# Kernel tuning notes

Measured on AMD Instinct MI355X. Metric: run time of the kernel, lower is better.

## Reference

```python
import jax, jax.numpy as jnp
import numpy as np

B, T, E, H = 16, 512, 1024, 512  # batch, seq_len, embedding_size_contactenated, contextualization_size


def setup_inputs() -> dict:
    key = jax.random.key(0)
    ks = jax.random.split(key, 10)
    s = 0.02
    return {
        "context_emb": jax.random.normal(ks[0], (B, T, E), dtype=jnp.float32),
        # coupled-gate LSTM cell: 3 gates (i, j, o); W: [3H, E+H]
        "w_fwd": jax.random.normal(ks[1], (3 * H, E + H), dtype=jnp.float32) * s,
        "b_fwd": jnp.zeros((3 * H,), dtype=jnp.float32),
        "w_bwd": jax.random.normal(ks[2], (3 * H, E + H), dtype=jnp.float32) * s,
        "b_bwd": jnp.zeros((3 * H,), dtype=jnp.float32),
        # learned initial states (xavier-ish), shape [1, H] each
        "h0_fwd": jax.random.normal(ks[3], (1, H), dtype=jnp.float32) * s,
        "h0_bwd": jax.random.normal(ks[4], (1, H), dtype=jnp.float32) * s,
        "c0_fwd": jax.random.normal(ks[5], (1, H), dtype=jnp.float32) * s,
        "c0_bwd": jax.random.normal(ks[6], (1, H), dtype=jnp.float32) * s,
    }


def _run_dir(x, w, b, h0, c0):
    # x: [T, B, E]; w: [3H, E+H]; h0, c0: [B, H]
    def step(carry, xt):
        h, c = carry
        gates = jnp.concatenate([xt, h], axis=-1) @ w.T + b  # [B, 3H]
        i, j, o = jnp.split(gates, 3, axis=-1)
        i = jax.nn.sigmoid(i)
        c = (1.0 - i) * c + i * jnp.tanh(j)  # coupled input/forget gate
        h = jnp.tanh(c) * jax.nn.sigmoid(o)
        return (h, c), h

    _, ys = jax.lax.scan(step, (h0, c0), x)
    return ys  # [T, B, H]


def reference(context_emb, w_fwd, b_fwd, w_bwd, b_bwd, h0_fwd, h0_bwd, c0_fwd, c0_bwd):
    x = jnp.transpose(context_emb, (1, 0, 2))  # [T, B, E] (time-major)
    batch = x.shape[1]
    rep = lambda s: jnp.tile(s, (batch, 1))  # repeat learned init state over batch
    out_f = _run_dir(x, w_fwd, b_fwd, rep(h0_fwd), rep(c0_fwd))
    out_b = _run_dir(x[::-1], w_bwd, b_bwd, rep(h0_bwd), rep(c0_bwd))[::-1]
    out = jnp.concatenate([out_f, out_b], axis=-1)  # [T, B, 2H]
    # dropout is identity in eval mode
    return jnp.transpose(out, (1, 0, 2))  # [B, T, 2H]
```

## Files before the change

kernel.cpp:

```cpp
#include <hip/hip_runtime.h>
#include <hip/hip_bf16.h>


typedef __attribute__((ext_vector_type(8))) short s8v;
typedef __attribute__((ext_vector_type(4))) short s4v;
typedef __attribute__((ext_vector_type(4))) float f4v;
typedef __attribute__((ext_vector_type(4))) unsigned short us4;
typedef unsigned long long u64;
typedef unsigned int u32;

#define XBF_OFF   0ull
#define WXBF_OFF  16777216ull
#define WHBF_OFF  23068672ull
#define XG_OFF    26214400ull
#define HST_OFF   76546048ull
#define TAG_OFF   76677120ull

static __device__ __forceinline__ short f2bf(float f) {
  __hip_bfloat16 h = __float2bfloat16(f);
  return *reinterpret_cast<short*>(&h);
}
static __device__ __forceinline__ float bf2f(unsigned short u) {
  union { unsigned int i; float f; } x;
  x.i = ((unsigned int)u) << 16;
  return x.f;
}
static __device__ __forceinline__ float sigmoidf_(float x) {
  return 1.0f / (1.0f + __expf(-x));
}
static __device__ __forceinline__ float tanhf_(float x) {
  return 1.0f - 2.0f / (1.0f + __expf(2.0f * x));
}

__global__ void init_state(const float* __restrict__ h0f, const float* __restrict__ h0b,
                           short* __restrict__ hst, u32* __restrict__ tags) {
  int i = blockIdx.x * 256 + threadIdx.x;
  if (i < 2 * 16 * 512) {
    int dir = i >> 13;
    int r = i & 8191;
    int col = r & 511;
    const float* h0 = dir ? h0b : h0f;
    hst[(size_t)dir * 4 * 8192 + r] = f2bf(h0[col]);
  }
  if (i < 64) tags[i] = 0;
}

__global__ void cast_x(const float* __restrict__ x, short* __restrict__ xb) {
  int i = (blockIdx.x * 256 + threadIdx.x) * 4;
  f4v v = *reinterpret_cast<const f4v*>(x + i);
  s4v o;
#pragma unroll
  for (int j = 0; j < 4; ++j) o[j] = f2bf(v[j]);
  *reinterpret_cast<s4v*>(xb + i) = o;
}

__global__ void cast_w(const float* __restrict__ wf, const float* __restrict__ wb,
                       short* __restrict__ wxb, short* __restrict__ whb) {
  int e = blockIdx.x * 256 + threadIdx.x;
  int dir = blockIdx.y;
  const float* w = dir ? wb : wf;
  int n = e / 1536;
  int k = e - n * 1536;
  short v = f2bf(w[e]);
  if (k < 1024)
    wxb[((size_t)(dir * 1536 + n)) * 1024 + k] = v;
  else
    whb[((size_t)(dir * 1536 + n)) * 512 + (k - 1024)] = v;
}

__global__ __launch_bounds__(256) void gemm_in(const short* __restrict__ Xb,
                                               const short* __restrict__ Wxb,
                                               short* __restrict__ Xg) {
  __shared__ short As[128 * 72];
  __shared__ short Bs[128 * 72];
  int tid = threadIdx.x;
  int lane = tid & 63;
  int lr = lane & 15, quad = lane >> 4;
  int widx = tid >> 6;
  int wr = widx >> 1, wc = widx & 1;
  int bm = blockIdx.x, bn = blockIdx.y;

  f4v acc[4][4];
#pragma unroll
  for (int a = 0; a < 4; ++a)
#pragma unroll
    for (int b = 0; b < 4; ++b) acc[a][b] = {0.f, 0.f, 0.f, 0.f};

  const short* Arow = Xb + (size_t)bm * 128 * 1024;
  const short* Brow = Wxb + (size_t)bn * 128 * 1024;

  for (int kt = 0; kt < 16; ++kt) {
#pragma unroll
    for (int c = 0; c < 4; ++c) {
      int fl = c * 2048 + tid * 8;
      int row = fl >> 6, col = fl & 63;
      *reinterpret_cast<s8v*>(&As[row * 72 + col]) =
          *reinterpret_cast<const s8v*>(Arow + row * 1024 + kt * 64 + col);
      *reinterpret_cast<s8v*>(&Bs[row * 72 + col]) =
          *reinterpret_cast<const s8v*>(Brow + row * 1024 + kt * 64 + col);
    }
    __syncthreads();
#pragma unroll
    for (int kk = 0; kk < 2; ++kk) {
      s8v af[4], bfv[4];
#pragma unroll
      for (int mi = 0; mi < 4; ++mi)
        af[mi] = *reinterpret_cast<const s8v*>(&As[(wr * 64 + mi * 16 + lr) * 72 + kk * 32 + quad * 8]);
#pragma unroll
      for (int ni = 0; ni < 4; ++ni)
        bfv[ni] = *reinterpret_cast<const s8v*>(&Bs[(wc * 64 + ni * 16 + lr) * 72 + kk * 32 + quad * 8]);
#pragma unroll
      for (int mi = 0; mi < 4; ++mi)
#pragma unroll
        for (int ni = 0; ni < 4; ++ni)
          acc[mi][ni] = __builtin_amdgcn_mfma_f32_16x16x32_bf16(af[mi], bfv[ni], acc[mi][ni], 0, 0, 0);
    }
    __syncthreads();
  }

  int ngbase = bn * 128;
  int dir = (ngbase >= 1536) ? 1 : 0;
  int ng0 = ngbase - dir * 1536;
#pragma unroll
  for (int mi = 0; mi < 4; ++mi) {
#pragma unroll
    for (int ni = 0; ni < 4; ++ni) {
      int colg = ng0 + wc * 64 + ni * 16 + lr;
#pragma unroll
      for (int r = 0; r < 4; ++r) {
        int m = bm * 128 + wr * 64 + mi * 16 + quad * 4 + r;
        int b = m >> 9, t = m & 511;
        Xg[(((size_t)(dir * 512 + t)) * 1536 + colg) * 16 + b] = f2bf(acc[mi][ni][r]);
      }
    }
  }
}

__global__ __launch_bounds__(64, 1) void lstm_rec(
    const short* __restrict__ Whb, const short* __restrict__ Xg,
    const float* __restrict__ bfw, const float* __restrict__ bbw,
    const float* __restrict__ c0f, const float* __restrict__ c0b,
    short* __restrict__ hst, u32* __restrict__ tags, float* __restrict__ out) {
  int lane = threadIdx.x & 63;
  int lr = lane & 15, quad = lane >> 4;
  int wg = blockIdx.x;
  int dir = wg >> 5;
  int slice = wg & 31;
  int col16 = slice * 16;

  const short* Whd = Whb + (size_t)dir * 1536 * 512;
  s8v Bw[3][16];
#pragma unroll
  for (int g = 0; g < 3; ++g) {
    const short* rp = Whd + (size_t)(g * 512 + col16 + lr) * 512 + quad * 8;
#pragma unroll
    for (int k = 0; k < 16; ++k) Bw[g][k] = *reinterpret_cast<const s8v*>(rp + k * 32);
  }

  const float* bias = dir ? bbw : bfw;
  float bi = bias[col16 + lr];
  float bj = bias[512 + col16 + lr];
  float bo = bias[1024 + col16 + lr];

  const float* c0 = dir ? c0b : c0f;
  float cst[4];
  {
    float c0v = c0[col16 + lr];
#pragma unroll
    for (int r = 0; r < 4; ++r) cst[r] = c0v;
  }

  short* hring = hst + (size_t)dir * 4 * 8192;
  u32* tg = tags + dir * 32;
  const short* xgbase = Xg + (size_t)dir * 512 * 1536 * 16;

  int t0 = dir ? 511 : 0;
  const short* xgp = xgbase + (size_t)t0 * 1536 * 16;
  us4 xiv = *reinterpret_cast<const us4*>(xgp + (col16 + lr) * 16 + quad * 4);
  us4 xjv = *reinterpret_cast<const us4*>(xgp + (512 + col16 + lr) * 16 + quad * 4);
  us4 xov = *reinterpret_cast<const us4*>(xgp + (1024 + col16 + lr) * 16 + quad * 4);

  for (int s = 0; s < 512; ++s) {
    int t = dir ? (511 - s) : s;

    for (;;) {
      int tv = (int)__hip_atomic_load(&tg[lane & 31], __ATOMIC_RELAXED,
                                      __HIP_MEMORY_SCOPE_AGENT);
      if (__ballot(tv >= s) == ~0ull) break;
    }

    const char* hp = (const char*)(hring + (size_t)(s & 3) * 8192) + lr * 1024 + quad * 16;
    s8v d0, d1, d2, d3, d4, d5, d6, d7, d8, d9, d10, d11, d12, d13, d14, d15;
    asm volatile(
        "global_load_dwordx4 %0, %16, off sc0 sc1\n\t"
        "global_load_dwordx4 %1, %16, off offset:64 sc0 sc1\n\t"
        "global_load_dwordx4 %2, %16, off offset:128 sc0 sc1\n\t"
        "global_load_dwordx4 %3, %16, off offset:192 sc0 sc1\n\t"
        "global_load_dwordx4 %4, %16, off offset:256 sc0 sc1\n\t"
        "global_load_dwordx4 %5, %16, off offset:320 sc0 sc1\n\t"
        "global_load_dwordx4 %6, %16, off offset:384 sc0 sc1\n\t"
        "global_load_dwordx4 %7, %16, off offset:448 sc0 sc1\n\t"
        "global_load_dwordx4 %8, %16, off offset:512 sc0 sc1\n\t"
        "global_load_dwordx4 %9, %16, off offset:576 sc0 sc1\n\t"
        "global_load_dwordx4 %10, %16, off offset:640 sc0 sc1\n\t"
        "global_load_dwordx4 %11, %16, off offset:704 sc0 sc1\n\t"
        "global_load_dwordx4 %12, %16, off offset:768 sc0 sc1\n\t"
        "global_load_dwordx4 %13, %16, off offset:832 sc0 sc1\n\t"
        "global_load_dwordx4 %14, %16, off offset:896 sc0 sc1\n\t"
        "global_load_dwordx4 %15, %16, off offset:960 sc0 sc1\n\t"
        "s_waitcnt vmcnt(0)"
        : "=v"(d0), "=v"(d1), "=v"(d2), "=v"(d3), "=v"(d4), "=v"(d5),
          "=v"(d6), "=v"(d7), "=v"(d8), "=v"(d9), "=v"(d10), "=v"(d11),
          "=v"(d12), "=v"(d13), "=v"(d14), "=v"(d15)
        : "v"(hp)
        : "memory");

    f4v a0 = {0.f, 0.f, 0.f, 0.f};
    f4v a1 = {0.f, 0.f, 0.f, 0.f};
    f4v a2 = {0.f, 0.f, 0.f, 0.f};
    s8v av[16] = {d0, d1, d2, d3, d4, d5, d6, d7, d8, d9, d10, d11, d12, d13, d14, d15};
#pragma unroll
    for (int k = 0; k < 16; ++k) {
      a0 = __builtin_amdgcn_mfma_f32_16x16x32_bf16(av[k], Bw[0][k], a0, 0, 0, 0);
      a1 = __builtin_amdgcn_mfma_f32_16x16x32_bf16(av[k], Bw[1][k], a1, 0, 0, 0);
      a2 = __builtin_amdgcn_mfma_f32_16x16x32_bf16(av[k], Bw[2][k], a2, 0, 0, 0);
    }

    float hn[4];
    u32 hv[4];
#pragma unroll
    for (int r = 0; r < 4; ++r) {
      float gi = a0[r] + bf2f(xiv[r]) + bi;
      float gj = a1[r] + bf2f(xjv[r]) + bj;
      float go = a2[r] + bf2f(xov[r]) + bo;
      float ii = sigmoidf_(gi);
      float jt = tanhf_(gj);
      float oo = sigmoidf_(go);
      cst[r] = (1.0f - ii) * cst[r] + ii * jt;
      hn[r] = tanhf_(cst[r]) * oo;
      hv[r] = (u32)(unsigned short)f2bf(hn[r]);
    }

    {
      short* hd = hring + (size_t)((s + 1) & 3) * 8192;
      const short* hsp = hd + (quad * 4) * 512 + col16 + lr;
      asm volatile(
          "global_store_short %4, %0, off sc0 sc1\n\t"
          "global_store_short %4, %1, off offset:1024 sc0 sc1\n\t"
          "global_store_short %4, %2, off offset:2048 sc0 sc1\n\t"
          "global_store_short %4, %3, off offset:3072 sc0 sc1\n\t"
          "s_waitcnt vmcnt(0)"
          :: "v"(hv[0]), "v"(hv[1]), "v"(hv[2]), "v"(hv[3]), "v"(hsp)
          : "memory");
      if (lane == 0)
        __hip_atomic_store(&tg[slice], (u32)(s + 1), __ATOMIC_RELAXED,
                           __HIP_MEMORY_SCOPE_AGENT);
    }

#pragma unroll
    for (int r = 0; r < 4; ++r)
      out[((size_t)(quad * 4 + r) * 512 + t) * 1024 + dir * 512 + col16 + lr] = hn[r];

    if (s < 511) {
      int tn = dir ? (511 - (s + 1)) : (s + 1);
      const short* xgn = xgbase + (size_t)tn * 1536 * 16;
      xiv = *reinterpret_cast<const us4*>(xgn + (col16 + lr) * 16 + quad * 4);
      xjv = *reinterpret_cast<const us4*>(xgn + (512 + col16 + lr) * 16 + quad * 4);
      xov = *reinterpret_cast<const us4*>(xgn + (1024 + col16 + lr) * 16 + quad * 4);
    }
  }
}

extern "C" void kernel_launch(void* const* d_in, const int* in_sizes, int n_in,
                              void* d_out, int out_size, void* d_ws, size_t ws_size,
                              hipStream_t stream) {
  const float* x    = (const float*)d_in[0];
  const float* wfw  = (const float*)d_in[1];
  const float* bfw  = (const float*)d_in[2];
  const float* wbw  = (const float*)d_in[3];
  const float* bbw  = (const float*)d_in[4];
  const float* h0f  = (const float*)d_in[5];
  const float* h0b  = (const float*)d_in[6];
  const float* c0f  = (const float*)d_in[7];
  const float* c0b  = (const float*)d_in[8];
  float* out = (float*)d_out;

  unsigned char* ws = (unsigned char*)d_ws;
  short* Xbf  = (short*)(ws + XBF_OFF);
  short* Wxbf = (short*)(ws + WXBF_OFF);
  short* Whbf = (short*)(ws + WHBF_OFF);
  short* Xg   = (short*)(ws + XG_OFF);
  short* hst  = (short*)(ws + HST_OFF);
  u32*   tags = (u32*)(ws + TAG_OFF);

  init_state<<<64, 256, 0, stream>>>(h0f, h0b, hst, tags);
  cast_x<<<8192, 256, 0, stream>>>(x, Xbf);
  cast_w<<<dim3(9216, 2), 256, 0, stream>>>(wfw, wbw, Wxbf, Whbf);
  gemm_in<<<dim3(64, 24), 256, 0, stream>>>(Xbf, Wxbf, Xg);
  lstm_rec<<<64, 64, 0, stream>>>(Whbf, Xg, bfw, bbw, c0f, c0b, hst, tags, out);
}
```

Before: 1.812 ms.

## Replace tag-based step barrier with step-stamped hidden-state words

Each bf16 hidden value is now stored in a 32-bit word whose high half carries the step number. Consumers poll the hidden-state buffer directly until every word shows the expected step, which removes the separate tag store, the tag polling loop and the store waitcnt. The ring shrinks from four buffers to two. In exchange, each poll reads twice as many bytes and unpacks them into MFMA operands, and correctness relies on each 32-bit store being atomic.

```diff
diff --git a/kernel.cpp b/kernel.cpp
--- a/kernel.cpp
+++ b/kernel.cpp
@@ -6,6 +6,7 @@
 typedef __attribute__((ext_vector_type(4))) short s4v;
 typedef __attribute__((ext_vector_type(4))) float f4v;
 typedef __attribute__((ext_vector_type(4))) unsigned short us4;
+typedef __attribute__((ext_vector_type(4))) unsigned int u4v;
 typedef unsigned long long u64;
 typedef unsigned int u32;
 
@@ -14,7 +15,6 @@
 #define WHBF_OFF  23068672ull
 #define XG_OFF    26214400ull
 #define HST_OFF   76546048ull
-#define TAG_OFF   76677120ull
 
 static __device__ __forceinline__ short f2bf(float f) {
   __hip_bfloat16 h = __float2bfloat16(f);
@@ -33,16 +33,17 @@
 }
 
 __global__ void init_state(const float* __restrict__ h0f, const float* __restrict__ h0b,
-                           short* __restrict__ hst, u32* __restrict__ tags) {
+                           u32* __restrict__ hst) {
   int i = blockIdx.x * 256 + threadIdx.x;
   if (i < 2 * 16 * 512) {
     int dir = i >> 13;
     int r = i & 8191;
     int col = r & 511;
     const float* h0 = dir ? h0b : h0f;
-    hst[(size_t)dir * 4 * 8192 + r] = f2bf(h0[col]);
-  }
-  if (i < 64) tags[i] = 0;
+    u32 v = (u32)(unsigned short)f2bf(h0[col]);
+    hst[(size_t)dir * 16384 + r] = v;
+    hst[(size_t)dir * 16384 + 8192 + r] = 0xFFFF0000u;
+  }
 }
 
 __global__ void cast_x(const float* __restrict__ x, short* __restrict__ xb) {
@@ -140,7 +141,7 @@
     const short* __restrict__ Whb, const short* __restrict__ Xg,
     const float* __restrict__ bfw, const float* __restrict__ bbw,
     const float* __restrict__ c0f, const float* __restrict__ c0b,
-    short* __restrict__ hst, u32* __restrict__ tags, float* __restrict__ out) {
+    u32* __restrict__ hst, float* __restrict__ out) {
   int lane = threadIdx.x & 63;
   int lr = lane & 15, quad = lane >> 4;
   int wg = blockIdx.x;
@@ -170,8 +171,7 @@
     for (int r = 0; r < 4; ++r) cst[r] = c0v;
   }
 
-  short* hring = hst + (size_t)dir * 4 * 8192;
-  u32* tg = tags + dir * 32;
+  u32* hring = hst + (size_t)dir * 16384;
   const short* xgbase = Xg + (size_t)dir * 512 * 1536 * 16;
 
   int t0 = dir ? 511 : 0;
@@ -182,43 +182,85 @@
 
   for (int s = 0; s < 512; ++s) {
     int t = dir ? (511 - s) : s;
-
+    u32 texp = (u32)s << 16;
+
+    const char* hp = (const char*)(hring + (size_t)(s & 1) * 8192) + lr * 2048 + quad * 32;
+    u4v e[32];
     for (;;) {
-      int tv = (int)__hip_atomic_load(&tg[lane & 31], __ATOMIC_RELAXED,
-                                      __HIP_MEMORY_SCOPE_AGENT);
-      if (__ballot(tv >= s) == ~0ull) break;
-    }
-
-    const char* hp = (const char*)(hring + (size_t)(s & 3) * 8192) + lr * 1024 + quad * 16;
-    s8v d0, d1, d2, d3, d4, d5, d6, d7, d8, d9, d10, d11, d12, d13, d14, d15;
-    asm volatile(
-        "global_load_dwordx4 %0, %16, off sc0 sc1\n\t"
-        "global_load_dwordx4 %1, %16, off offset:64 sc0 sc1\n\t"
-        "global_load_dwordx4 %2, %16, off offset:128 sc0 sc1\n\t"
-        "global_load_dwordx4 %3, %16, off offset:192 sc0 sc1\n\t"
-        "global_load_dwordx4 %4, %16, off offset:256 sc0 sc1\n\t"
-        "global_load_dwordx4 %5, %16, off offset:320 sc0 sc1\n\t"
-        "global_load_dwordx4 %6, %16, off offset:384 sc0 sc1\n\t"
-        "global_load_dwordx4 %7, %16, off offset:448 sc0 sc1\n\t"
-        "global_load_dwordx4 %8, %16, off offset:512 sc0 sc1\n\t"
-        "global_load_dwordx4 %9, %16, off offset:576 sc0 sc1\n\t"
-        "global_load_dwordx4 %10, %16, off offset:640 sc0 sc1\n\t"
-        "global_load_dwordx4 %11, %16, off offset:704 sc0 sc1\n\t"
-        "global_load_dwordx4 %12, %16, off offset:768 sc0 sc1\n\t"
-        "global_load_dwordx4 %13, %16, off offset:832 sc0 sc1\n\t"
-        "global_load_dwordx4 %14, %16, off offset:896 sc0 sc1\n\t"
-        "global_load_dwordx4 %15, %16, off offset:960 sc0 sc1\n\t"
-        "s_waitcnt vmcnt(0)"
-        : "=v"(d0), "=v"(d1), "=v"(d2), "=v"(d3), "=v"(d4), "=v"(d5),
-          "=v"(d6), "=v"(d7), "=v"(d8), "=v"(d9), "=v"(d10), "=v"(d11),
-          "=v"(d12), "=v"(d13), "=v"(d14), "=v"(d15)
-        : "v"(hp)
-        : "memory");
+      asm volatile(
+          "global_load_dwordx4 %0, %16, off sc0 sc1\n\t"
+          "global_load_dwordx4 %1, %16, off offset:16 sc0 sc1\n\t"
+          "global_load_dwordx4 %2, %16, off offset:128 sc0 sc1\n\t"
+          "global_load_dwordx4 %3, %16, off offset:144 sc0 sc1\n\t"
+          "global_load_dwordx4 %4, %16, off offset:256 sc0 sc1\n\t"
+          "global_load_dwordx4 %5, %16, off offset:272 sc0 sc1\n\t"
+          "global_load_dwordx4 %6, %16, off offset:384 sc0 sc1\n\t"
+          "global_load_dwordx4 %7, %16, off offset:400 sc0 sc1\n\t"
+          "global_load_dwordx4 %8, %16, off offset:512 sc0 sc1\n\t"
+          "global_load_dwordx4 %9, %16, off offset:528 sc0 sc1\n\t"
+          "global_load_dwordx4 %10, %16, off offset:640 sc0 sc1\n\t"
+          "global_load_dwordx4 %11, %16, off offset:656 sc0 sc1\n\t"
+          "global_load_dwordx4 %12, %16, off offset:768 sc0 sc1\n\t"
+          "global_load_dwordx4 %13, %16, off offset:784 sc0 sc1\n\t"
+          "global_load_dwordx4 %14, %16, off offset:896 sc0 sc1\n\t"
+          "global_load_dwordx4 %15, %16, off offset:912 sc0 sc1"
+          : "=v"(e[0]), "=v"(e[1]), "=v"(e[2]), "=v"(e[3]), "=v"(e[4]),
+            "=v"(e[5]), "=v"(e[6]), "=v"(e[7]), "=v"(e[8]), "=v"(e[9]),
+            "=v"(e[10]), "=v"(e[11]), "=v"(e[12]), "=v"(e[13]), "=v"(e[14]),
+            "=v"(e[15])
+          : "v"(hp)
+          : "memory");
+      asm volatile(
+          "global_load_dwordx4 %0, %16, off offset:1024 sc0 sc1\n\t"
+          "global_load_dwordx4 %1, %16, off offset:1040 sc0 sc1\n\t"
+          "global_load_dwordx4 %2, %16, off offset:1152 sc0 sc1\n\t"
+          "global_load_dwordx4 %3, %16, off offset:1168 sc0 sc1\n\t"
+          "global_load_dwordx4 %4, %16, off offset:1280 sc0 sc1\n\t"
+          "global_load_dwordx4 %5, %16, off offset:1296 sc0 sc1\n\t"
+          "global_load_dwordx4 %6, %16, off offset:1408 sc0 sc1\n\t"
+          "global_load_dwordx4 %7, %16, off offset:1424 sc0 sc1\n\t"
+          "global_load_dwordx4 %8, %16, off offset:1536 sc0 sc1\n\t"
+          "global_load_dwordx4 %9, %16, off offset:1552 sc0 sc1\n\t"
+          "global_load_dwordx4 %10, %16, off offset:1664 sc0 sc1\n\t"
+          "global_load_dwordx4 %11, %16, off offset:1680 sc0 sc1\n\t"
+          "global_load_dwordx4 %12, %16, off offset:1792 sc0 sc1\n\t"
+          "global_load_dwordx4 %13, %16, off offset:1808 sc0 sc1\n\t"
+          "global_load_dwordx4 %14, %16, off offset:1920 sc0 sc1\n\t"
+          "global_load_dwordx4 %15, %16, off offset:1936 sc0 sc1\n\t"
+          "s_waitcnt vmcnt(0)"
+          : "=v"(e[16]), "=v"(e[17]), "=v"(e[18]), "=v"(e[19]), "=v"(e[20]),
+            "=v"(e[21]), "=v"(e[22]), "=v"(e[23]), "=v"(e[24]), "=v"(e[25]),
+            "=v"(e[26]), "=v"(e[27]), "=v"(e[28]), "=v"(e[29]), "=v"(e[30]),
+            "=v"(e[31])
+          : "v"(hp)
+          : "memory");
+      __builtin_amdgcn_sched_barrier(0);
+      u32 diff = 0;
+#pragma unroll
+      for (int q = 0; q < 32; ++q) {
+#pragma unroll
+        for (int j = 0; j < 4; ++j) diff |= (e[q][j] ^ texp) & 0xFFFF0000u;
+      }
+      if (__ballot(diff == 0) == ~0ull) break;
+    }
+
+    s8v av[16];
+#pragma unroll
+    for (int k = 0; k < 16; ++k) {
+      u4v lo = e[2 * k], hi = e[2 * k + 1];
+      u4v p;
+      p[0] = (lo[0] & 0xFFFFu) | (lo[1] << 16);
+      p[1] = (lo[2] & 0xFFFFu) | (lo[3] << 16);
+      p[2] = (hi[0] & 0xFFFFu) | (hi[1] << 16);
+      p[3] = (hi[2] & 0xFFFFu) | (hi[3] << 16);
+      union { u4v u; s8v s; } cv;
+      cv.u = p;
+      av[k] = cv.s;
+    }
 
     f4v a0 = {0.f, 0.f, 0.f, 0.f};
     f4v a1 = {0.f, 0.f, 0.f, 0.f};
     f4v a2 = {0.f, 0.f, 0.f, 0.f};
-    s8v av[16] = {d0, d1, d2, d3, d4, d5, d6, d7, d8, d9, d10, d11, d12, d13, d14, d15};
 #pragma unroll
     for (int k = 0; k < 16; ++k) {
       a0 = __builtin_amdgcn_mfma_f32_16x16x32_bf16(av[k], Bw[0][k], a0, 0, 0, 0);
@@ -228,6 +270,7 @@
 
     float hn[4];
     u32 hv[4];
+    u32 st = ((u32)(s + 1)) << 16;
 #pragma unroll
     for (int r = 0; r < 4; ++r) {
       float gi = a0[r] + bf2f(xiv[r]) + bi;
@@ -238,23 +281,19 @@
       float oo = sigmoidf_(go);
       cst[r] = (1.0f - ii) * cst[r] + ii * jt;
       hn[r] = tanhf_(cst[r]) * oo;
-      hv[r] = (u32)(unsigned short)f2bf(hn[r]);
+      hv[r] = st | (u32)(unsigned short)f2bf(hn[r]);
     }
 
     {
-      short* hd = hring + (size_t)((s + 1) & 3) * 8192;
-      const short* hsp = hd + (quad * 4) * 512 + col16 + lr;
+      u32* hd0 = hring + (size_t)((s + 1) & 1) * 8192 + (quad * 4) * 512 + col16 + lr;
+      u32* hd2 = hd0 + 1024;
       asm volatile(
-          "global_store_short %4, %0, off sc0 sc1\n\t"
-          "global_store_short %4, %1, off offset:1024 sc0 sc1\n\t"
-          "global_store_short %4, %2, off offset:2048 sc0 sc1\n\t"
-          "global_store_short %4, %3, off offset:3072 sc0 sc1\n\t"
-          "s_waitcnt vmcnt(0)"
-          :: "v"(hv[0]), "v"(hv[1]), "v"(hv[2]), "v"(hv[3]), "v"(hsp)
+          "global_store_dword %4, %0, off sc0 sc1\n\t"
+          "global_store_dword %4, %1, off offset:2048 sc0 sc1\n\t"
+          "global_store_dword %5, %2, off sc0 sc1\n\t"
+          "global_store_dword %5, %3, off offset:2048 sc0 sc1"
+          :: "v"(hv[0]), "v"(hv[1]), "v"(hv[2]), "v"(hv[3]), "v"(hd0), "v"(hd2)
           : "memory");
-      if (lane == 0)
-        __hip_atomic_store(&tg[slice], (u32)(s + 1), __ATOMIC_RELAXED,
-                           __HIP_MEMORY_SCOPE_AGENT);
     }
 
 #pragma unroll
@@ -290,12 +329,11 @@
   short* Wxbf = (short*)(ws + WXBF_OFF);
   short* Whbf = (short*)(ws + WHBF_OFF);
   short* Xg   = (short*)(ws + XG_OFF);
-  short* hst  = (short*)(ws + HST_OFF);
-  u32*   tags = (u32*)(ws + TAG_OFF);
-
-  init_state<<<64, 256, 0, stream>>>(h0f, h0b, hst, tags);
+  u32*   hst  = (u32*)(ws + HST_OFF);
+
+  init_state<<<64, 256, 0, stream>>>(h0f, h0b, hst);
   cast_x<<<8192, 256, 0, stream>>>(x, Xbf);
   cast_w<<<dim3(9216, 2), 256, 0, stream>>>(wfw, wbw, Wxbf, Whbf);
   gemm_in<<<dim3(64, 24), 256, 0, stream>>>(Xbf, Wxbf, Xg);
-  lstm_rec<<<64, 64, 0, stream>>>(Whbf, Xg, bfw, bbw, c0f, c0b, hst, tags, out);
-}
+  lstm_rec<<<64, 64, 0, stream>>>(Whbf, Xg, bfw, bbw, c0f, c0b, hst, out);
+}
```

New measurement: 3.463 ms. 1.91x slower.
